# Kernel tuning notes

Hardware: AMD Instinct MI355X
Metric: run time of the kernel (lower is better)

The kernel has to match this reference:

```python
import math
import jax, jax.numpy as jnp
import numpy as np

L, B, S, D, HID, NH = 4, 2, 2048, 1024, 1024, 16
C = HID // NH  # 64


def setup_inputs() -> dict:
    key = jax.random.key(0)
    ks = jax.random.split(key, 8)
    p = lambda k, shape: jax.random.normal(k, shape, jnp.float32) * 0.02
    return {
        "x": jax.random.normal(ks[0], (B, S, D), jnp.float32),
        "Wq": p(ks[1], (L, D, HID)), "bq": jnp.zeros((L, HID), jnp.float32),
        "Wk": p(ks[2], (L, D, HID)), "bk": jnp.zeros((L, HID), jnp.float32),
        "Wv": p(ks[3], (L, D, HID)), "bv": jnp.zeros((L, HID), jnp.float32),
        "Wo": p(ks[4], (L, HID, D)), "bo": jnp.zeros((L, D), jnp.float32),
        "W1": p(ks[5], (L, D, HID)), "b1": jnp.zeros((L, HID), jnp.float32),
        "W2": p(ks[6], (L, HID, D)), "b2": jnp.zeros((L, D), jnp.float32),
        "gamma": jnp.ones((L, D), jnp.float32),   # single LayerNorm reused twice per block
        "beta": jnp.zeros((L, D), jnp.float32),
    }


def _pos_enc(seq_len, d, n=1000.0):
    col = jnp.arange(seq_len, dtype=jnp.float32)[:, None]        # [S,1]
    row = jnp.arange(d)                                          # [D]
    exp = (2.0 * (row // 2).astype(jnp.float32)) / d
    mat = col / jnp.power(n, exp)[None, :]                       # [S,D]
    return jnp.where(row % 2 == 0, jnp.sin(mat), jnp.cos(mat))


def _layernorm(x, g, b, eps=1e-5):
    mu = jnp.mean(x, axis=-1, keepdims=True)
    var = jnp.mean((x - mu) ** 2, axis=-1, keepdims=True)        # biased, as torch
    return (x - mu) / jnp.sqrt(var + eps) * g + b


def _block(x, Wq, bq, Wk, bk, Wv, bv, Wo, bo, W1, b1, W2, b2, g, be):
    b_, s_, _ = x.shape
    q = ((x @ Wq + bq)).reshape(b_, s_, NH, C) / math.sqrt(C)
    k = (x @ Wk + bk).reshape(b_, s_, NH, C)
    v = (x @ Wv + bv).reshape(b_, s_, NH, C)
    # NOTE: faithful to original einsum '...hq,...hk->...hqk' -> per-token
    # attention over the CHANNEL axis c, with a (c,c) causal mask.
    aff = jnp.einsum('bshq,bshk->bshqk', q, k)                   # [B,S,H,C,C]
    mask = jnp.triu(jnp.ones((C, C), bool), 1)
    aff = jnp.where(mask, -jnp.inf, aff)
    w = jax.nn.softmax(aff, axis=-1)
    av = jnp.einsum('bshqk,bshk->bshq', w, v).reshape(b_, s_, HID)
    attn_out = av @ Wo + bo
    x = _layernorm(attn_out + x, g, be)
    mlp_out = jax.nn.relu(x @ W1 + b1) @ W2 + b2
    return _layernorm(mlp_out + x, g, be)


def reference(x, Wq, bq, Wk, bk, Wv, bv, Wo, bo, W1, b1, W2, b2, gamma, beta):
    x = x + _pos_enc(x.shape[1], x.shape[2])
    for i in range(L):
        x = _block(x, Wq[i], bq[i], Wk[i], bk[i], Wv[i], bv[i], Wo[i], bo[i],
                   W1[i], b1[i], W2[i], b2[i], gamma[i], beta[i])
    return x
```

## Files before the change

kernel.cpp:

```cpp
#include <hip/hip_runtime.h>
#include <hip/hip_bf16.h>
#include <stdint.h>

#define TOK 4096
#define DM  1024

using u16 = unsigned short;
typedef __attribute__((ext_vector_type(8))) short short8;
typedef __attribute__((ext_vector_type(4))) float f32x4;

__device__ __forceinline__ u16 f2bf(float f){
  unsigned u = __float_as_uint(f);
  return (u16)((u + 0x7fffu + ((u >> 16) & 1u)) >> 16);
}
__device__ __forceinline__ float bf2f(u16 h){ return __uint_as_float(((unsigned)h) << 16); }

__device__ __forceinline__ float fexp2(float x){
#if __has_builtin(__builtin_amdgcn_exp2f)
  return __builtin_amdgcn_exp2f(x);
#else
  float r; asm("v_exp_f32 %0, %1\n\ts_nop 0" : "=v"(r) : "v"(x)); return r;
#endif
}
__device__ __forceinline__ float frcp(float x){
#if __has_builtin(__builtin_amdgcn_rcpf)
  return __builtin_amdgcn_rcpf(x);
#else
  float r; asm("v_rcp_f32 %0, %1\n\ts_nop 0" : "=v"(r) : "v"(x)); return r;
#endif
}

__global__ __launch_bounds__(256) void posenc_add(
    const float* __restrict__ x, u16* __restrict__ xb)
{
  const int t = blockIdx.x;
  const int s = t & 2047;
  const size_t base = (size_t)t * DM;
#pragma unroll
  for (int i = 0; i < 4; ++i){
    const int d = threadIdx.x + i * 256;
    const float e = (float)(d & ~1) * (1.0f / (float)DM);
    const float denom = powf(1000.0f, e);
    const float mat = (float)s / denom;
    const float pe = (d & 1) ? cosf(mat) : sinf(mat);
    xb[base + d] = f2bf(x[base + d] + pe);
  }
}

__global__ __launch_bounds__(256) void transpose6(
    const float* __restrict__ Wq, const float* __restrict__ Wk, const float* __restrict__ Wv,
    const float* __restrict__ Wo, const float* __restrict__ W1, const float* __restrict__ W2,
    u16* __restrict__ WT, int l0)
{
  __shared__ float tile[64 * 65];
  const int bid = blockIdx.x;
  const int l   = l0 + bid / 1536;
  const int rem = bid % 1536;
  const int mm  = rem >> 8;
  const int t   = rem & 255;
  const int tn  = (t & 15) * 64;
  const int tk  = (t >> 4) * 64;
  const float* src = (mm==0)?Wq:(mm==1)?Wk:(mm==2)?Wv:(mm==3)?Wo:(mm==4)?W1:W2;
  src += (size_t)l * 1048576;
  u16* dst = WT + ((size_t)(l - l0) * 6 + mm) * 1048576;
  const int tx = threadIdx.x & 15, ty = threadIdx.x >> 4;
#pragma unroll
  for (int r = 0; r < 4; ++r){
    const int row = ty + 16 * r;
    const float4 v = *(const float4*)(src + (size_t)(tk + row) * 1024 + tn + 4 * tx);
    tile[(4*tx + 0) * 65 + row] = v.x;
    tile[(4*tx + 1) * 65 + row] = v.y;
    tile[(4*tx + 2) * 65 + row] = v.z;
    tile[(4*tx + 3) * 65 + row] = v.w;
  }
  __syncthreads();
#pragma unroll
  for (int r = 0; r < 4; ++r){
    const int nrow = ty + 16 * r;
    ushort4 o;
    o.x = f2bf(tile[nrow * 65 + 4*tx + 0]);
    o.y = f2bf(tile[nrow * 65 + 4*tx + 1]);
    o.z = f2bf(tile[nrow * 65 + 4*tx + 2]);
    o.w = f2bf(tile[nrow * 65 + 4*tx + 3]);
    *(ushort4*)(dst + (size_t)(tn + nrow) * 1024 + tk + 4 * tx) = o;
  }
}

#define BM 128
#define BK 64
#define KD 1024

template<int MODE>
__global__ __launch_bounds__(256, 3) void gemm_k1024(
    const u16* __restrict__ A, const u16* __restrict__ BT,
    const float* __restrict__ bias0, const float* __restrict__ bias1, const float* __restrict__ bias2,
    u16* __restrict__ outB, int M, int N)
{
  constexpr int BNt = 64;
  constexpr int NFR = 2;
  __shared__ __align__(16) u16 lds2[2][(BM + BNt) * BK];
  const int tid  = threadIdx.x;
  const int lane = tid & 63;
  const int wave = tid >> 6;
  const int nbn = N / BNt;
  const int nwg = gridDim.x;
  const int wg  = (blockIdx.x & 7) * (nwg >> 3) + (blockIdx.x >> 3);
  const size_t m0 = (size_t)(wg / nbn) * BM;
  const size_t n0 = (size_t)(wg % nbn) * BNt;

  const int srow  = lane >> 3;
  const int sslot = (lane & 7) ^ srow;
  const u16* gA = A  + (m0 + wave*32 + srow) * KD + sslot * 8;
  const u16* gB = BT + (n0 + wave*16 + srow) * KD + sslot * 8;
  const int loA = (wave*32) * 64;
  const int loB = BM*BK + (wave*16) * 64;

  const int wm = (wave >> 1) * 64;
  const int wn = (wave & 1) * 32;
  f32x4 acc[4][NFR] = {};

  auto stage = [&](int kt, int buf){
    u16* base = lds2[buf];
    const int k0 = kt * BK;
#pragma unroll
    for (int p = 0; p < 4; ++p)
      __builtin_amdgcn_global_load_lds(
          (const __attribute__((address_space(1))) void*)(gA + p*8*KD + k0),
          (__attribute__((address_space(3))) void*)(base + loA + p*512), 16, 0, 0);
#pragma unroll
    for (int p = 0; p < 2; ++p)
      __builtin_amdgcn_global_load_lds(
          (const __attribute__((address_space(1))) void*)(gB + p*8*KD + k0),
          (__attribute__((address_space(3))) void*)(base + loB + p*512), 16, 0, 0);
  };
  auto compute = [&](int buf){
    const u16* sAc = lds2[buf];
    const u16* sBc = sAc + BM*BK;
#pragma unroll
    for (int kk = 0; kk < 2; ++kk){
      short8 af[4], bfr[NFR];
      const int kidx = kk*4 + (lane >> 4);
#pragma unroll
      for (int i = 0; i < 4; ++i){
        const int arow = wm + i*16 + (lane & 15);
        af[i]  = *(const short8*)(sAc + arow*64 + (kidx ^ (arow & 7)) * 8);
      }
#pragma unroll
      for (int j = 0; j < NFR; ++j){
        const int brow = wn + j*16 + (lane & 15);
        bfr[j] = *(const short8*)(sBc + brow*64 + (kidx ^ (brow & 7)) * 8);
      }
#pragma unroll
      for (int i = 0; i < 4; ++i)
#pragma unroll
        for (int j = 0; j < NFR; ++j)
          acc[i][j] = __builtin_amdgcn_mfma_f32_16x16x32_bf16(af[i], bfr[j], acc[i][j], 0, 0, 0);
    }
  };

  stage(0, 0);
  __syncthreads();
  for (int kt = 0; kt < KD/BK; ++kt){
    if (kt + 1 < KD/BK) stage(kt + 1, (kt + 1) & 1);
    compute(kt & 1);
    __syncthreads();
  }

#pragma unroll
  for (int i = 0; i < 4; ++i){
    const int growb = wm + i*16 + (lane >> 4) * 4;
#pragma unroll
    for (int j = 0; j < NFR; ++j){
      const size_t gcol = n0 + wn + j*16 + (lane & 15);
      float bv;
      if constexpr (MODE == 2)
        bv = (gcol < 1024) ? bias0[gcol] : (gcol < 2048) ? bias1[gcol - 1024] : bias2[gcol - 2048];
      else
        bv = bias0[gcol];
#pragma unroll
      for (int r = 0; r < 4; ++r){
        const size_t grow = m0 + growb + r;
        float v = acc[i][j][r] + bv;
        if constexpr (MODE == 1) v = fmaxf(v, 0.0f);
        if constexpr (MODE == 2){ if (gcol < 1024) v *= 0.125f; }
        outB[grow * N + gcol] = f2bf(v);
      }
    }
  }
}

__global__ __launch_bounds__(256) void attn_chan(
    const u16* __restrict__ qkv, u16* __restrict__ av)
{
  __shared__ __align__(16) float2 skv[4][2][64];
  const int t    = blockIdx.x >> 1;
  const int lane = threadIdx.x & 63;
  const int wave = threadIdx.x >> 6;
  const int h0   = (blockIdx.x & 1) * 8 + wave * 2;
  const int r3   = lane & 3;
  const size_t base = (size_t)t * 3072 + h0 * 64 + lane;
  const float q0 = bf2f(qkv[base])      * 1.44269504f;
  const float q1 = bf2f(qkv[base + 64]) * 1.44269504f;
  skv[wave][0][lane] = make_float2(bf2f(qkv[base + 1024]), bf2f(qkv[base + 2048]));
  skv[wave][1][lane] = make_float2(bf2f(qkv[base + 1088]), bf2f(qkv[base + 2112]));
  const float2* kwa = skv[wave][0];
  const float2* kwb = skv[wave][1];
  float sa0=0.f, sa1=0.f, aa0=0.f, aa1=0.f;
  float sb0=0.f, sb1=0.f, ab0=0.f, ab1=0.f;
#pragma unroll
  for (int j0 = 0; j0 < 64; j0 += 4){
    const float4 A0 = *(const float4*)(kwa + j0);
    const float4 A1 = *(const float4*)(kwa + j0 + 2);
    const float4 B0 = *(const float4*)(kwb + j0);
    const float4 B1 = *(const float4*)(kwb + j0 + 2);
    const float bias = (j0 + 3 <= lane) ? 0.0f : -200.0f;
    const float ea0 = fexp2(fmaf(q0, A0.x, bias));
    const float ea1 = fexp2(fmaf(q0, A0.z, bias));
    const float ea2 = fexp2(fmaf(q0, A1.x, bias));
    const float ea3 = fexp2(fmaf(q0, A1.z, bias));
    const float eb0 = fexp2(fmaf(q1, B0.x, bias));
    const float eb1 = fexp2(fmaf(q1, B0.z, bias));
    const float eb2 = fexp2(fmaf(q1, B1.x, bias));
    const float eb3 = fexp2(fmaf(q1, B1.z, bias));
    sa0 += ea0 + ea2;  sa1 += ea1 + ea3;
    sb0 += eb0 + eb2;  sb1 += eb1 + eb3;
    aa0 = fmaf(ea0, A0.y, fmaf(ea2, A1.y, aa0));
    aa1 = fmaf(ea1, A0.w, fmaf(ea3, A1.w, aa1));
    ab0 = fmaf(eb0, B0.y, fmaf(eb2, B1.y, ab0));
    ab1 = fmaf(eb1, B0.w, fmaf(eb3, B1.w, ab1));
  }
#pragma unroll
  for (int s = 0; s < 3; ++s){
    const int jj = lane - r3 + s;
    const float bias = (s <= r3 && r3 < 3) ? 0.0f : -200.0f;
    const float2 ka = kwa[jj];
    const float2 kb = kwb[jj];
    const float ea = fexp2(fmaf(q0, ka.x, bias));
    const float eb = fexp2(fmaf(q1, kb.x, bias));
    sa0 += ea; aa0 = fmaf(ea, ka.y, aa0);
    sb0 += eb; ab0 = fmaf(eb, kb.y, ab0);
  }
  av[(size_t)t * DM + h0*64 + lane]      = f2bf((aa0 + aa1) * frcp(sa0 + sa1));
  av[(size_t)t * DM + h0*64 + 64 + lane] = f2bf((ab0 + ab1) * frcp(sb0 + sb1));
}

__global__ __launch_bounds__(256) void residual_ln(
    const u16* __restrict__ y, const u16* xres,
    const float* __restrict__ gamma, const float* __restrict__ beta,
    float* xoutF, u16* xb)
{
  const int lane = threadIdx.x & 63, wave = threadIdx.x >> 6;
  const int row  = blockIdx.x * 4 + wave;
  const ushort4* yr = (const ushort4*)(y    + (size_t)row*DM);
  const ushort4* xr = (const ushort4*)(xres + (size_t)row*DM);
  float4 s[4];
  float psum = 0.0f;
#pragma unroll
  for (int c = 0; c < 4; ++c){
    const int idx = c*64 + lane;
    const ushort4 a = yr[idx];
    const ushort4 b = xr[idx];
    s[c].x = bf2f(a.x)+bf2f(b.x); s[c].y = bf2f(a.y)+bf2f(b.y);
    s[c].z = bf2f(a.z)+bf2f(b.z); s[c].w = bf2f(a.w)+bf2f(b.w);
    psum += (s[c].x + s[c].y) + (s[c].z + s[c].w);
  }
#pragma unroll
  for (int o = 32; o; o >>= 1) psum += __shfl_xor(psum, o);
  const float mu = psum * (1.0f/(float)DM);
  float q2 = 0.0f;
#pragma unroll
  for (int c = 0; c < 4; ++c){
    s[c].x -= mu; s[c].y -= mu; s[c].z -= mu; s[c].w -= mu;
    q2 += s[c].x*s[c].x + s[c].y*s[c].y + s[c].z*s[c].z + s[c].w*s[c].w;
  }
#pragma unroll
  for (int o = 32; o; o >>= 1) q2 += __shfl_xor(q2, o);
  const float rstd = rsqrtf(q2 * (1.0f/(float)DM) + 1e-5f);
#pragma unroll
  for (int c = 0; c < 4; ++c){
    const int idx = c*64 + lane;
    const float4 g  = ((const float4*)gamma)[idx];
    const float4 be = ((const float4*)beta)[idx];
    float4 o4;
    o4.x = s[c].x*rstd*g.x + be.x;
    o4.y = s[c].y*rstd*g.y + be.y;
    o4.z = s[c].z*rstd*g.z + be.z;
    o4.w = s[c].w*rstd*g.w + be.w;
    if (xoutF) ((float4*)(xoutF + (size_t)row*DM))[idx] = o4;
    ushort4 ob; ob.x=f2bf(o4.x); ob.y=f2bf(o4.y); ob.z=f2bf(o4.z); ob.w=f2bf(o4.w);
    ((ushort4*)(xb + (size_t)row*DM))[idx] = ob;
  }
}

extern "C" void kernel_launch(void* const* d_in, const int* in_sizes, int n_in,
                              void* d_out, int out_size, void* d_ws, size_t ws_size,
                              hipStream_t stream)
{
  const float* x    = (const float*)d_in[0];
  const float* Wq   = (const float*)d_in[1];
  const float* bq   = (const float*)d_in[2];
  const float* Wk   = (const float*)d_in[3];
  const float* bk   = (const float*)d_in[4];
  const float* Wv   = (const float*)d_in[5];
  const float* bv   = (const float*)d_in[6];
  const float* Wo   = (const float*)d_in[7];
  const float* bo   = (const float*)d_in[8];
  const float* W1   = (const float*)d_in[9];
  const float* b1   = (const float*)d_in[10];
  const float* W2   = (const float*)d_in[11];
  const float* b2   = (const float*)d_in[12];
  const float* gam  = (const float*)d_in[13];
  const float* bet  = (const float*)d_in[14];

  char* ws = (char*)d_ws;
  size_t off = 0;
  auto alloc = [&](size_t b){ void* p = ws + off; off = (off + b + 255) & ~(size_t)255; return p; };

  const size_t oneWT = 6ull*1048576*2;
  const size_t rest  = ((size_t)TOK*DM*2)
                     + ((size_t)TOK*3072*2)
                     + ((size_t)TOK*DM*2)
                     + ((size_t)TOK*DM*2)
                     + ((size_t)TOK*DM*2)
                     + 4096;
  const bool all4 = (4*oneWT + rest) <= ws_size;

  u16*   WT   = (u16*)  alloc(all4 ? 4*oneWT : oneWT);
  u16*   xb   = (u16*)  alloc((size_t)TOK*DM*2);
  u16*   qkv  = (u16*)  alloc((size_t)TOK*3072*2);
  u16*   avb  = (u16*)  alloc((size_t)TOK*DM*2);
  u16*   hbuf = (u16*)  alloc((size_t)TOK*DM*2);
  u16*   ybuf = (u16*)  alloc((size_t)TOK*DM*2);
  if (off > ws_size) return;

  posenc_add<<<TOK, 256, 0, stream>>>(x, xb);
  if (all4)
    transpose6<<<4*1536, 256, 0, stream>>>(Wq, Wk, Wv, Wo, W1, W2, WT, 0);

  for (int l = 0; l < 4; ++l){
    u16* wt = all4 ? (WT + (size_t)l * 6 * 1048576) : WT;
    if (!all4)
      transpose6<<<1536, 256, 0, stream>>>(Wq, Wk, Wv, Wo, W1, W2, WT, l);
    gemm_k1024<2><<<(TOK/BM)*(3072/64), 256, 0, stream>>>(
        xb, wt, bq + l*1024, bk + l*1024, bv + l*1024, qkv, TOK, 3072);
    attn_chan<<<TOK*2, 256, 0, stream>>>(qkv, avb);
    gemm_k1024<0><<<(TOK/BM)*(1024/64), 256, 0, stream>>>(
        avb, wt + 3ull*1048576, bo + l*1024, nullptr, nullptr, ybuf, TOK, 1024);
    residual_ln<<<TOK/4, 256, 0, stream>>>(ybuf, xb, gam + l*1024, bet + l*1024, nullptr, xb);
    gemm_k1024<1><<<(TOK/BM)*(1024/64), 256, 0, stream>>>(
        xb, wt + 4ull*1048576, b1 + l*1024, nullptr, nullptr, hbuf, TOK, 1024);
    gemm_k1024<0><<<(TOK/BM)*(1024/64), 256, 0, stream>>>(
        hbuf, wt + 5ull*1048576, b2 + l*1024, nullptr, nullptr, ybuf, TOK, 1024);
    residual_ln<<<TOK/4, 256, 0, stream>>>(ybuf, xb, gam + l*1024, bet + l*1024,
                                           (l == 3) ? (float*)d_out : nullptr, xb);
  }
}
```

Measured before the change: 557.3 us.

## Add dedicated 256x192-tile, 8-wave QKV GEMM with interleaved prefetch and priority

Replaces the generic 128x64-tile QKV projection with a specialized 512-thread kernel using 256x192 tiles. Staging of the next K slice is interleaved with the MFMA phases, and s_setprio raises priority around the MFMA bursts. Larger tiles raise arithmetic intensity and cut global/LDS traffic per FLOP. The cost is more registers and LDS per workgroup, lower occupancy, and only 256 workgroups to spread across the CUs.

```diff
diff --git a/kernel.cpp b/kernel.cpp
--- a/kernel.cpp
+++ b/kernel.cpp
@@ -90,10 +90,124 @@
 #define BK 64
 #define KD 1024
 
+#define QBM 256
+#define QBN 192
+#define QNT (KD/BK)
+
+__global__ __launch_bounds__(512, 2) void qkv_gemm8(
+    const u16* __restrict__ A, const u16* __restrict__ BT,
+    const float* __restrict__ bq, const float* __restrict__ bk, const float* __restrict__ bvp,
+    u16* __restrict__ outB)
+{
+  __shared__ __align__(16) u16 lds[2][(QBM + QBN) * BK];
+  const int tid  = threadIdx.x;
+  const int lane = tid & 63;
+  const int wave = tid >> 6;
+  const int nwg  = gridDim.x;
+  const int wg   = (blockIdx.x & 7) * (nwg >> 3) + (blockIdx.x >> 3);
+  const int nbn  = 3072 / QBN;
+  const size_t m0 = (size_t)(wg / nbn) * QBM;
+  const size_t n0 = (size_t)(wg % nbn) * QBN;
+
+  const int srow  = lane >> 3;
+  const int sslot = (lane & 7) ^ srow;
+  const u16* gA = A  + (m0 + wave*32 + srow) * KD + sslot * 8;
+  const u16* gB = BT + (n0 + wave*24 + srow) * KD + sslot * 8;
+  const int loA = wave * 32 * 64;
+  const int loB = QBM * BK + wave * 24 * 64;
+
+  auto stage1 = [&](int kt, int buf, int i){
+    const int k0 = kt * BK;
+    if (i < 4)
+      __builtin_amdgcn_global_load_lds(
+          (const __attribute__((address_space(1))) void*)(gA + i*8*KD + k0),
+          (__attribute__((address_space(3))) void*)(&lds[buf][loA + i*512]), 16, 0, 0);
+    else
+      __builtin_amdgcn_global_load_lds(
+          (const __attribute__((address_space(1))) void*)(gB + (i-4)*8*KD + k0),
+          (__attribute__((address_space(3))) void*)(&lds[buf][loB + (i-4)*512]), 16, 0, 0);
+  };
+
+  const int wr = wave >> 2;
+  const int wc = wave & 3;
+  f32x4 acc[8][3] = {};
+  short8 bfv[3][2];
+
+#pragma unroll
+  for (int i = 0; i < 7; ++i) stage1(0, 0, i);
+
+  for (int kt = 0; kt < QNT; ++kt){
+    const int cur = kt & 1;
+    asm volatile("s_waitcnt vmcnt(0)" ::: "memory");
+    __builtin_amdgcn_sched_barrier(0);
+    __builtin_amdgcn_s_barrier();
+    const u16* sA = &lds[cur][0];
+    const u16* sB = &lds[cur][QBM * BK];
+#pragma unroll
+    for (int p = 0; p < 4; ++p){
+      short8 af[2][2];
+#pragma unroll
+      for (int i = 0; i < 2; ++i)
+#pragma unroll
+        for (int kh = 0; kh < 2; ++kh){
+          const int ar = wr*128 + (p*2 + i)*16 + (lane & 15);
+          af[i][kh] = *(const short8*)(sA + ar*64 + ((((kh<<2)|(lane>>4)) ^ (ar & 7)) * 8));
+        }
+      if (p == 0){
+#pragma unroll
+        for (int j = 0; j < 3; ++j)
+#pragma unroll
+          for (int kh = 0; kh < 2; ++kh){
+            const int br = wc*48 + j*16 + (lane & 15);
+            bfv[j][kh] = *(const short8*)(sB + br*64 + ((((kh<<2)|(lane>>4)) ^ (br & 7)) * 8));
+          }
+      }
+      if (kt + 1 < QNT){
+        stage1(kt + 1, cur ^ 1, p*2);
+        if (p*2 + 1 < 7) stage1(kt + 1, cur ^ 1, p*2 + 1);
+      }
+      __builtin_amdgcn_s_barrier();
+      asm volatile("s_waitcnt lgkmcnt(0)" ::: "memory");
+      __builtin_amdgcn_sched_barrier(0);
+      __builtin_amdgcn_s_setprio(1);
+#pragma unroll
+      for (int i = 0; i < 2; ++i)
+#pragma unroll
+        for (int j = 0; j < 3; ++j)
+#pragma unroll
+          for (int kh = 0; kh < 2; ++kh)
+            acc[p*2 + i][j] = __builtin_amdgcn_mfma_f32_16x16x32_bf16(
+                af[i][kh], bfv[j][kh], acc[p*2 + i][j], 0, 0, 0);
+      __builtin_amdgcn_s_setprio(0);
+      __builtin_amdgcn_s_barrier();
+    }
+  }
+
+#pragma unroll
+  for (int m = 0; m < 8; ++m){
+    const int growb = wr*128 + m*16 + (lane >> 4) * 4;
+#pragma unroll
+    for (int j = 0; j < 3; ++j){
+      const size_t gcol = n0 + wc*48 + j*16 + (lane & 15);
+      float bias;
+      if (gcol < 1024)      bias = bq[gcol];
+      else if (gcol < 2048) bias = bk[gcol - 1024];
+      else                  bias = bvp[gcol - 2048];
+#pragma unroll
+      for (int r = 0; r < 4; ++r){
+        const size_t grow = m0 + growb + r;
+        float v = acc[m][j][r] + bias;
+        if (gcol < 1024) v *= 0.125f;
+        outB[grow * 3072 + gcol] = f2bf(v);
+      }
+    }
+  }
+}
+
 template<int MODE>
 __global__ __launch_bounds__(256, 3) void gemm_k1024(
     const u16* __restrict__ A, const u16* __restrict__ BT,
-    const float* __restrict__ bias0, const float* __restrict__ bias1, const float* __restrict__ bias2,
+    const float* __restrict__ bias0,
     u16* __restrict__ outB, int M, int N)
 {
   constexpr int BNt = 64;
@@ -172,17 +286,12 @@
 #pragma unroll
     for (int j = 0; j < NFR; ++j){
       const size_t gcol = n0 + wn + j*16 + (lane & 15);
-      float bv;
-      if constexpr (MODE == 2)
-        bv = (gcol < 1024) ? bias0[gcol] : (gcol < 2048) ? bias1[gcol - 1024] : bias2[gcol - 2048];
-      else
-        bv = bias0[gcol];
+      const float bv = bias0[gcol];
 #pragma unroll
       for (int r = 0; r < 4; ++r){
         const size_t grow = m0 + growb + r;
         float v = acc[i][j][r] + bv;
         if constexpr (MODE == 1) v = fmaxf(v, 0.0f);
-        if constexpr (MODE == 2){ if (gcol < 1024) v *= 0.125f; }
         outB[grow * N + gcol] = f2bf(v);
       }
     }
@@ -341,16 +450,16 @@
     u16* wt = all4 ? (WT + (size_t)l * 6 * 1048576) : WT;
     if (!all4)
       transpose6<<<1536, 256, 0, stream>>>(Wq, Wk, Wv, Wo, W1, W2, WT, l);
-    gemm_k1024<2><<<(TOK/BM)*(3072/64), 256, 0, stream>>>(
-        xb, wt, bq + l*1024, bk + l*1024, bv + l*1024, qkv, TOK, 3072);
+    qkv_gemm8<<<(TOK/QBM)*(3072/QBN), 512, 0, stream>>>(
+        xb, wt, bq + l*1024, bk + l*1024, bv + l*1024, qkv);
     attn_chan<<<TOK*2, 256, 0, stream>>>(qkv, avb);
     gemm_k1024<0><<<(TOK/BM)*(1024/64), 256, 0, stream>>>(
-        avb, wt + 3ull*1048576, bo + l*1024, nullptr, nullptr, ybuf, TOK, 1024);
+        avb, wt + 3ull*1048576, bo + l*1024, ybuf, TOK, 1024);
     residual_ln<<<TOK/4, 256, 0, stream>>>(ybuf, xb, gam + l*1024, bet + l*1024, nullptr, xb);
     gemm_k1024<1><<<(TOK/BM)*(1024/64), 256, 0, stream>>>(
-        xb, wt + 4ull*1048576, b1 + l*1024, nullptr, nullptr, hbuf, TOK, 1024);
+        xb, wt + 4ull*1048576, b1 + l*1024, hbuf, TOK, 1024);
     gemm_k1024<0><<<(TOK/BM)*(1024/64), 256, 0, stream>>>(
-        hbuf, wt + 5ull*1048576, b2 + l*1024, nullptr, nullptr, ybuf, TOK, 1024);
+        hbuf, wt + 5ull*1048576, b2 + l*1024, ybuf, TOK, 1024);
     residual_ln<<<TOK/4, 256, 0, stream>>>(ybuf, xb, gam + l*1024, bet + l*1024,
                                            (l == 3) ? (float*)d_out : nullptr, xb);
   }
```

Result: faster. 536.2 us (median of 2 runs) (-3.8%).
